# Kernel optimization log

Measured on AMD Instinct MI355X. Metric: run time of the kernel, lower is better.

The kernel has to match this reference:

```python
import jax, jax.numpy as jnp
import numpy as np

B, T, D, H, L = 8, 128, 400, 300, 45  # batch, max_length, 2*word_lstm_size, hidden, tag_count


def setup_inputs() -> dict:
    key = jax.random.key(0)
    ks = jax.random.split(key, 10)
    s = 0.05
    return {
        "cont_repr": jax.random.normal(ks[0], (B, T, D), jnp.float32),
        "root": jax.random.normal(ks[1], (1, 1, D), jnp.float32),
        "W1a": jax.random.normal(ks[2], (D, H), jnp.float32) * s,
        "W1b": jax.random.normal(ks[3], (D, H), jnp.float32) * s,
        "b1": jnp.zeros((H,), jnp.float32),
        "Wa": jax.random.normal(ks[4], (H, 1), jnp.float32) * s,
        "ba": jnp.zeros((1,), jnp.float32),
        "Wl": jax.random.normal(ks[5], (H, L), jnp.float32) * s,
        "bl": jnp.zeros((L,), jnp.float32),
        "sentence_lengths": jax.random.randint(ks[6], (B,), 0, T + 1),
        "desired_arcs": jax.random.randint(ks[7], (B, T), 0, T + 1),
        "desired_labels": jax.random.randint(ks[8], (B, T), 0, L),
        "use_desired_arcs": 1,
    }


def reference(cont_repr, root, W1a, W1b, b1, Wa, ba, Wl, bl,
              sentence_lengths, desired_arcs, desired_labels, use_desired_arcs):
    b, t, d = cont_repr.shape
    mask = (jnp.arange(t)[None, :] < sentence_lengths[:, None]).astype(cont_repr.dtype)  # [B,T]
    n_valid = jnp.maximum(mask.sum(), 1.0)

    # Dense(concat(tile_a, tile_b)) == tile_a @ W1a + tile_b @ W1b (exact same math,
    # avoids materializing the [B,T,T+1,2D] concat the TF graph builds).
    a_proj = jnp.einsum('btd,dh->bth', cont_repr, W1a)                     # [B,T,H]
    with_root = jnp.concatenate([jnp.broadcast_to(root, (b, 1, d)), cont_repr], axis=1)  # [B,T+1,D]
    b_proj = jnp.einsum('bsd,dh->bsh', with_root, W1b)                     # [B,T+1,H]
    h = jax.nn.relu(a_proj[:, :, None, :] + b_proj[:, None, :, :] + b1)    # [B,T,T+1,H]

    # UAS: arc scorer (units=1) over T+1 head candidates
    arc_logits = jnp.einsum('btsh,ho->btso', h, Wa)[..., 0] + ba[0]        # [B,T,T+1]
    predicted_arcs = jnp.argmax(arc_logits, axis=-1)                        # [B,T]
    arc_logp = jax.nn.log_softmax(arc_logits, axis=-1)
    arc_ce = -jnp.take_along_axis(arc_logp, desired_arcs[..., None], axis=-1)[..., 0]
    uas_loss = (arc_ce * mask).sum() / n_valid

    # LAS: gather pair repr at selected head, score labels
    sel = desired_arcs if use_desired_arcs else predicted_arcs             # [B,T]
    idx = jnp.broadcast_to(sel[:, :, None, None], (b, t, 1, h.shape[-1]))
    sel_h = jnp.take_along_axis(h, idx, axis=2)[:, :, 0, :]                # [B,T,H]
    lab_logits = jnp.einsum('bth,hl->btl', sel_h, Wl) + bl                 # [B,T,L]
    lab_logp = jax.nn.log_softmax(lab_logits, axis=-1)
    lab_ce = -jnp.take_along_axis(lab_logp, desired_labels[..., None], axis=-1)[..., 0]
    las_loss = (lab_ce * mask).sum() / n_valid

    return (uas_loss + las_loss) / 2
```

## Files before the change

kernel.cpp:

```cpp
#include <hip/hip_runtime.h>
#include <hip/hip_bf16.h>
#include <math.h>

#define BN 8
#define TT 128
#define DD 400
#define HH 300
#define LL 45
#define KH 200
#define SS 129
#define ALG_STRIDE 132
#define PADW 308

__global__ __launch_bounds__(640) void proj_kernel(
    const float* __restrict__ cont, const float* __restrict__ root,
    const float* __restrict__ W1a, const float* __restrict__ W1b,
    const float* __restrict__ b1,
    const int* __restrict__ slen,
    float* __restrict__ AP, float* __restrict__ BPX,
    float* __restrict__ accum)
{
    __shared__ float red[320][9];
    const int blk = blockIdx.x;
    const int tid = threadIdx.x;
    const int grp = tid / 320;
    const int h   = tid % 320;
    const int d0  = __builtin_amdgcn_readfirstlane(grp * KH);

    if (blk == 256) {
        if (tid == 0) accum[0] = 0.f;
        float acc = 0.f;
        if (h < HH) {
            const float* wp = W1b + (size_t)d0 * HH + h;
            for (int d = 0; d < KH; ++d)
                acc = fmaf(root[d0 + d], wp[(size_t)d * HH], acc);
        }
        if (grp == 1) red[h][0] = acc;
        __syncthreads();
        if (grp == 0 && h < HH) {
            const float v = acc + red[h][0];
            for (int bb = 0; bb < BN; ++bb)
                BPX[(size_t)bb * SS * HH + h] = v;
        }
        return;
    }

    const bool isA = (blk < 128);
    const int rb   = isA ? blk : blk - 128;
    const int row0 = rb * 8;
    if (isA) {
        const int lenb = slen[row0 >> 7];
        if ((row0 & 127) >= lenb) return;
    }

    const float* W    = isA ? W1a : W1b;
    const float* rows = cont + (size_t)row0 * DD + d0;

    float acc[8];
    #pragma unroll
    for (int r = 0; r < 8; ++r) acc[r] = 0.f;

    if (h < HH) {
        const float* wp = W + (size_t)d0 * HH + h;
        float w[8];
        #pragma unroll
        for (int k = 0; k < 8; ++k) w[k] = wp[(size_t)k * HH];
        for (int dc = 0; dc < KH; dc += 8) {
            float wn[8];
            if (dc + 8 < KH) {
                #pragma unroll
                for (int k = 0; k < 8; ++k) wn[k] = wp[(size_t)(dc + 8 + k) * HH];
            } else {
                #pragma unroll
                for (int k = 0; k < 8; ++k) wn[k] = 0.f;
            }
            #pragma unroll
            for (int r = 0; r < 8; ++r) {
                const float* rp = rows + r * DD + dc;
                #pragma unroll
                for (int k = 0; k < 8; ++k)
                    acc[r] = fmaf(rp[k], w[k], acc[r]);
            }
            #pragma unroll
            for (int k = 0; k < 8; ++k) w[k] = wn[k];
        }
    }

    if (grp == 1) {
        #pragma unroll
        for (int r = 0; r < 8; ++r) red[h][r] = acc[r];
    }
    __syncthreads();
    if (grp == 0 && h < HH) {
        if (isA) {
            const float bb = b1[h];
            float* dst = AP + (size_t)row0 * HH + h;
            #pragma unroll
            for (int r = 0; r < 8; ++r)
                dst[(size_t)r * HH] = acc[r] + red[h][r] + bb;
        } else {
            const int b = row0 >> 7, t = row0 & 127;
            float* dst = BPX + ((size_t)(b * SS + t + 1)) * HH + h;
            #pragma unroll
            for (int r = 0; r < 8; ++r)
                dst[(size_t)r * HH] = acc[r] + red[h][r];
        }
    }
}

__global__ __launch_bounds__(256) void arc_kernel(
    const float* __restrict__ AP, const float* __restrict__ BPX,
    const float* __restrict__ Wa, const int* __restrict__ slen,
    float* __restrict__ ALG)
{
    __shared__ float ap_s[8][PADW];
    __shared__ float bp_s[33][PADW];
    __shared__ float wa_s[PADW];

    const int blk = blockIdx.x;
    const int b  = blk >> 6;
    const int tt = (blk >> 2) & 15;
    const int sc = blk & 3;
    const int t0 = tt * 8;
    if (t0 >= slen[b]) return;

    const int tid  = threadIdx.x;
    const int lane = tid & 63;
    const int wave = tid >> 6;
    const int tl   = lane & 7;
    const int sl   = lane >> 3;
    const int s0   = sc * 32;

    {
        const float* apg = AP + (size_t)(b * TT + t0) * HH;
        for (int i = tid; i < 8 * HH; i += 256)
            ap_s[i / HH][i % HH] = apg[(i / HH) * HH + i % HH];
        const float* bpg = BPX + (size_t)(b * SS + s0) * HH;
        for (int i = tid; i < 33 * HH; i += 256)
            bp_s[i / HH][i % HH] = bpg[(i / HH) * HH + i % HH];
        for (int i = tid; i < HH; i += 256)
            wa_s[i] = Wa[i];
    }
    __syncthreads();

    const int s_local = wave * 8 + sl;
    const float* aprow = ap_s[tl];
    const float* bprow = bp_s[s_local];

    float acc = 0.f;
    #pragma unroll 5
    for (int hh = 0; hh < HH; hh += 4) {
        const float4 a4 = *(const float4*)&aprow[hh];
        const float4 p4 = *(const float4*)&bprow[hh];
        const float4 w4 = *(const float4*)&wa_s[hh];
        acc = fmaf(fmaxf(a4.x + p4.x, 0.f), w4.x, acc);
        acc = fmaf(fmaxf(a4.y + p4.y, 0.f), w4.y, acc);
        acc = fmaf(fmaxf(a4.z + p4.z, 0.f), w4.z, acc);
        acc = fmaf(fmaxf(a4.w + p4.w, 0.f), w4.w, acc);
    }
    ALG[(size_t)(b * TT + t0 + tl) * ALG_STRIDE + s0 + s_local] = acc;

    if (sc == 3 && wave == 0 && sl == 0) {
        const float* bpr = bp_s[32];
        float a2 = 0.f;
        #pragma unroll 5
        for (int hh = 0; hh < HH; hh += 4) {
            const float4 a4 = *(const float4*)&aprow[hh];
            const float4 p4 = *(const float4*)&bpr[hh];
            const float4 w4 = *(const float4*)&wa_s[hh];
            a2 = fmaf(fmaxf(a4.x + p4.x, 0.f), w4.x, a2);
            a2 = fmaf(fmaxf(a4.y + p4.y, 0.f), w4.y, a2);
            a2 = fmaf(fmaxf(a4.z + p4.z, 0.f), w4.z, a2);
            a2 = fmaf(fmaxf(a4.w + p4.w, 0.f), w4.w, a2);
        }
        ALG[(size_t)(b * TT + t0 + tl) * ALG_STRIDE + 128] = a2;
    }
}

__global__ __launch_bounds__(256) void smx_kernel(
    const float* __restrict__ AP, const float* __restrict__ BPX,
    const float* __restrict__ Wl, const float* __restrict__ bl,
    const float* __restrict__ ALG,
    const int* __restrict__ slen, const int* __restrict__ des_arcs,
    const int* __restrict__ des_labels, const int* __restrict__ use_des,
    float* __restrict__ accum)
{
    const int blk = blockIdx.x;
    const int b = blk >> 7, t = blk & 127;
    if (t >= slen[b]) return;
    const int tid  = threadIdx.x;
    const int lane = tid & 63;
    const int wave = tid >> 6;

    __shared__ float selh[HH];
    __shared__ float partial[4][64];
    __shared__ float arc_ce_s;
    __shared__ int   sel_s;

    if (wave == 0) {
        const float* lg = ALG + (size_t)blk * ALG_STRIDE;
        const float v0 = lg[lane];
        const float v1 = lg[64 + lane];
        const float v2 = (lane == 0) ? lg[128] : -INFINITY;

        float m = fmaxf(fmaxf(v0, v1), v2);
        #pragma unroll
        for (int off = 32; off; off >>= 1) m = fmaxf(m, __shfl_xor(m, off, 64));
        float e = __expf(v0 - m) + __expf(v1 - m) + ((lane == 0) ? __expf(v2 - m) : 0.f);
        #pragma unroll
        for (int off = 32; off; off >>= 1) e += __shfl_xor(e, off, 64);
        const float arc_lse = m + __logf(e);

        float bv = v0; int bi = lane;
        if (v1 > bv) { bv = v1; bi = 64 + lane; }
        if (lane == 0 && v2 > bv) { bv = v2; bi = 128; }
        #pragma unroll
        for (int off = 32; off; off >>= 1) {
            const float ov = __shfl_xor(bv, off, 64);
            const int   oi = __shfl_xor(bi, off, 64);
            if (ov > bv || (ov == bv && oi < bi)) { bv = ov; bi = oi; }
        }
        if (lane == 0) {
            const int da = des_arcs[b * TT + t];
            arc_ce_s = arc_lse - lg[da];
            sel_s = use_des[0] ? da : bi;
        }
    }
    __syncthreads();

    {
        const int sel = sel_s;
        const float* ap = AP + (size_t)blk * HH;
        const float* bp = BPX + (size_t)(b * SS + sel) * HH;
        for (int hh = tid; hh < HH; hh += 256)
            selh[hh] = fmaxf(ap[hh] + bp[hh], 0.f);
    }
    __syncthreads();

    {
        float p = 0.f;
        if (lane < LL) {
            const int h0 = wave * 75;
            #pragma unroll 5
            for (int j = 0; j < 75; ++j)
                p = fmaf(selh[h0 + j], Wl[(h0 + j) * LL + lane], p);
        }
        partial[wave][lane] = p;
    }
    __syncthreads();

    if (wave == 0) {
        float a = -INFINITY;
        if (lane < LL)
            a = bl[lane] + partial[0][lane] + partial[1][lane]
                         + partial[2][lane] + partial[3][lane];
        float lm = a;
        #pragma unroll
        for (int off = 32; off; off >>= 1) lm = fmaxf(lm, __shfl_xor(lm, off, 64));
        float le = (lane < LL) ? __expf(a - lm) : 0.f;
        #pragma unroll
        for (int off = 32; off; off >>= 1) le += __shfl_xor(le, off, 64);
        const float lab_lse = lm + __logf(le);

        const int dl = des_labels[b * TT + t];
        const float ldl = __shfl(a, dl, 64);
        if (lane == 0)
            atomicAdd(accum, arc_ce_s + (lab_lse - ldl));
    }
}

__global__ void finalize_kernel(const float* __restrict__ accum,
                                const int* __restrict__ slen,
                                float* __restrict__ out)
{
    if (threadIdx.x == 0) {
        int n = 0;
        for (int b = 0; b < BN; ++b) {
            int l = slen[b];
            if (l < 0) l = 0;
            if (l > TT) l = TT;
            n += l;
        }
        float nv = (float)n;
        if (nv < 1.f) nv = 1.f;
        out[0] = accum[0] / (2.f * nv);
    }
}

extern "C" void kernel_launch(void* const* d_in, const int* in_sizes, int n_in,
                              void* d_out, int out_size, void* d_ws, size_t ws_size,
                              hipStream_t stream) {
    const float* cont = (const float*)d_in[0];
    const float* root = (const float*)d_in[1];
    const float* W1a  = (const float*)d_in[2];
    const float* W1b  = (const float*)d_in[3];
    const float* b1   = (const float*)d_in[4];
    const float* Wa   = (const float*)d_in[5];
    const float* Wl   = (const float*)d_in[7];
    const float* bl   = (const float*)d_in[8];
    const int* slen   = (const int*)d_in[9];
    const int* darc   = (const int*)d_in[10];
    const int* dlab   = (const int*)d_in[11];
    const int* used   = (const int*)d_in[12];
    float* out = (float*)d_out;

    float* AP    = (float*)d_ws;
    float* BPX   = AP  + 1024 * HH;
    float* ALG   = BPX + BN * SS * HH;
    float* accum = ALG + 1024 * ALG_STRIDE;

    proj_kernel<<<257, 640, 0, stream>>>(cont, root, W1a, W1b, b1, slen, AP, BPX, accum);
    arc_kernel<<<512, 256, 0, stream>>>(AP, BPX, Wa, slen, ALG);
    smx_kernel<<<1024, 256, 0, stream>>>(AP, BPX, Wl, bl, ALG, slen, darc, dlab, used, accum);
    finalize_kernel<<<1, 64, 0, stream>>>(accum, slen, out);
}
```

Baseline: 47.11 us.

## Repartition projection kernel into more, smaller blocks without split-K reduction

Result: slower. 54.43 us (+15.5%).

```diff
diff --git a/kernel.cpp b/kernel.cpp
--- a/kernel.cpp
+++ b/kernel.cpp
@@ -7,12 +7,11 @@
 #define DD 400
 #define HH 300
 #define LL 45
-#define KH 200
 #define SS 129
 #define ALG_STRIDE 132
 #define PADW 308
 
-__global__ __launch_bounds__(640) void proj_kernel(
+__global__ __launch_bounds__(256) void proj_kernel(
     const float* __restrict__ cont, const float* __restrict__ root,
     const float* __restrict__ W1a, const float* __restrict__ W1b,
     const float* __restrict__ b1,
@@ -20,90 +19,85 @@
     float* __restrict__ AP, float* __restrict__ BPX,
     float* __restrict__ accum)
 {
-    __shared__ float red[320][9];
-    const int blk = blockIdx.x;
-    const int tid = threadIdx.x;
-    const int grp = tid / 320;
-    const int h   = tid % 320;
-    const int d0  = __builtin_amdgcn_readfirstlane(grp * KH);
-
-    if (blk == 256) {
+    const int tid  = threadIdx.x;
+    const int blk  = blockIdx.x;
+
+    if (blk == 1280) {
         if (tid == 0) accum[0] = 0.f;
-        float acc = 0.f;
-        if (h < HH) {
-            const float* wp = W1b + (size_t)d0 * HH + h;
-            for (int d = 0; d < KH; ++d)
-                acc = fmaf(root[d0 + d], wp[(size_t)d * HH], acc);
-        }
-        if (grp == 1) red[h][0] = acc;
-        __syncthreads();
-        if (grp == 0 && h < HH) {
-            const float v = acc + red[h][0];
+        for (int h = tid; h < HH; h += 256) {
+            float a0 = 0.f, a1 = 0.f, a2 = 0.f, a3 = 0.f;
+            const float* wp = W1b + h;
+            for (int d = 0; d < DD; d += 4) {
+                a0 = fmaf(root[d],     wp[(size_t)d * HH],           a0);
+                a1 = fmaf(root[d + 1], wp[(size_t)(d + 1) * HH],     a1);
+                a2 = fmaf(root[d + 2], wp[(size_t)(d + 2) * HH],     a2);
+                a3 = fmaf(root[d + 3], wp[(size_t)(d + 3) * HH],     a3);
+            }
+            const float v = (a0 + a1) + (a2 + a3);
+            #pragma unroll
             for (int bb = 0; bb < BN; ++bb)
                 BPX[(size_t)bb * SS * HH + h] = v;
         }
         return;
     }
 
-    const bool isA = (blk < 128);
-    const int rb   = isA ? blk : blk - 128;
+    const bool isA = (blk < 640);
+    const int q    = isA ? blk : blk - 640;
+    const int rb   = q / 5;
+    const int hc   = q % 5;
     const int row0 = rb * 8;
     if (isA) {
         const int lenb = slen[row0 >> 7];
         if ((row0 & 127) >= lenb) return;
     }
 
-    const float* W    = isA ? W1a : W1b;
-    const float* rows = cont + (size_t)row0 * DD + d0;
-
-    float acc[8];
+    const int lane = tid & 63;
+    const int wave = tid >> 6;
+    const int h    = hc * 64 + lane;
+    const bool hok = (h < HH);
+    const int hs   = hok ? h : 0;
+
+    const int roff = __builtin_amdgcn_readfirstlane((row0 + wave * 2) * DD);
+    const float* x0 = cont + roff;
+    const float* x1 = x0 + DD;
+
+    const float* wp = (isA ? W1a : W1b) + hs;
+
+    float acc0 = 0.f, acc1 = 0.f;
+    float w[8];
     #pragma unroll
-    for (int r = 0; r < 8; ++r) acc[r] = 0.f;
-
-    if (h < HH) {
-        const float* wp = W + (size_t)d0 * HH + h;
-        float w[8];
-        #pragma unroll
-        for (int k = 0; k < 8; ++k) w[k] = wp[(size_t)k * HH];
-        for (int dc = 0; dc < KH; dc += 8) {
-            float wn[8];
-            if (dc + 8 < KH) {
-                #pragma unroll
-                for (int k = 0; k < 8; ++k) wn[k] = wp[(size_t)(dc + 8 + k) * HH];
-            } else {
-                #pragma unroll
-                for (int k = 0; k < 8; ++k) wn[k] = 0.f;
-            }
+    for (int k = 0; k < 8; ++k) w[k] = wp[(size_t)k * HH];
+
+    for (int dc = 0; dc < DD; dc += 8) {
+        float wn[8];
+        if (dc + 8 < DD) {
             #pragma unroll
-            for (int r = 0; r < 8; ++r) {
-                const float* rp = rows + r * DD + dc;
-                #pragma unroll
-                for (int k = 0; k < 8; ++k)
-                    acc[r] = fmaf(rp[k], w[k], acc[r]);
-            }
+            for (int k = 0; k < 8; ++k) wn[k] = wp[(size_t)(dc + 8 + k) * HH];
+        } else {
             #pragma unroll
-            for (int k = 0; k < 8; ++k) w[k] = wn[k];
-        }
-    }
-
-    if (grp == 1) {
-        #pragma unroll
-        for (int r = 0; r < 8; ++r) red[h][r] = acc[r];
-    }
-    __syncthreads();
-    if (grp == 0 && h < HH) {
+            for (int k = 0; k < 8; ++k) wn[k] = 0.f;
+        }
+        #pragma unroll
+        for (int k = 0; k < 8; ++k) {
+            acc0 = fmaf(x0[dc + k], w[k], acc0);
+            acc1 = fmaf(x1[dc + k], w[k], acc1);
+        }
+        #pragma unroll
+        for (int k = 0; k < 8; ++k) w[k] = wn[k];
+    }
+
+    if (hok) {
+        const int t = (row0 & 127) + wave * 2;
         if (isA) {
             const float bb = b1[h];
-            float* dst = AP + (size_t)row0 * HH + h;
-            #pragma unroll
-            for (int r = 0; r < 8; ++r)
-                dst[(size_t)r * HH] = acc[r] + red[h][r] + bb;
+            float* dst = AP + (size_t)(row0 + wave * 2) * HH + h;
+            dst[0]  = acc0 + bb;
+            dst[HH] = acc1 + bb;
         } else {
-            const int b = row0 >> 7, t = row0 & 127;
+            const int b = row0 >> 7;
             float* dst = BPX + ((size_t)(b * SS + t + 1)) * HH + h;
-            #pragma unroll
-            for (int r = 0; r < 8; ++r)
-                dst[(size_t)r * HH] = acc[r] + red[h][r];
+            dst[0]  = acc0;
+            dst[HH] = acc1;
         }
     }
 }
@@ -309,7 +303,7 @@
     float* ALG   = BPX + BN * SS * HH;
     float* accum = ALG + 1024 * ALG_STRIDE;
 
-    proj_kernel<<<257, 640, 0, stream>>>(cont, root, W1a, W1b, b1, slen, AP, BPX, accum);
+    proj_kernel<<<1281, 256, 0, stream>>>(cont, root, W1a, W1b, b1, slen, AP, BPX, accum);
     arc_kernel<<<512, 256, 0, stream>>>(AP, BPX, Wa, slen, ALG);
     smx_kernel<<<1024, 256, 0, stream>>>(AP, BPX, Wl, bl, ALG, slen, darc, dlab, used, accum);
     finalize_kernel<<<1, 64, 0, stream>>>(accum, slen, out);
```

## Stage input rows in LDS and drop split-K reduction in projection kernel

Applied to the files above, without the earlier changes.

Result: slower. 58.12 us (+23.4%).

```diff
diff --git a/kernel.cpp b/kernel.cpp
--- a/kernel.cpp
+++ b/kernel.cpp
@@ -7,12 +7,11 @@
 #define DD 400
 #define HH 300
 #define LL 45
-#define KH 200
 #define SS 129
 #define ALG_STRIDE 132
 #define PADW 308
 
-__global__ __launch_bounds__(640) void proj_kernel(
+__global__ __launch_bounds__(320) void proj_kernel(
     const float* __restrict__ cont, const float* __restrict__ root,
     const float* __restrict__ W1a, const float* __restrict__ W1b,
     const float* __restrict__ b1,
@@ -20,91 +19,102 @@
     float* __restrict__ AP, float* __restrict__ BPX,
     float* __restrict__ accum)
 {
-    __shared__ float red[320][9];
+    __shared__ float rows_s[8 * DD];
     const int blk = blockIdx.x;
     const int tid = threadIdx.x;
-    const int grp = tid / 320;
-    const int h   = tid % 320;
-    const int d0  = __builtin_amdgcn_readfirstlane(grp * KH);
+    const int h   = tid;
+    const bool hok = (h < HH);
 
     if (blk == 256) {
         if (tid == 0) accum[0] = 0.f;
-        float acc = 0.f;
-        if (h < HH) {
-            const float* wp = W1b + (size_t)d0 * HH + h;
-            for (int d = 0; d < KH; ++d)
-                acc = fmaf(root[d0 + d], wp[(size_t)d * HH], acc);
-        }
-        if (grp == 1) red[h][0] = acc;
+        for (int i = tid; i < DD; i += 320) rows_s[i] = root[i];
         __syncthreads();
-        if (grp == 0 && h < HH) {
-            const float v = acc + red[h][0];
+        if (hok) {
+            const float* wp = W1b + h;
+            float acc = 0.f;
+            float w[8];
+            #pragma unroll
+            for (int k = 0; k < 8; ++k) w[k] = wp[(size_t)k * HH];
+            for (int dc = 0; dc < DD; dc += 8) {
+                float wn[8];
+                if (dc + 8 < DD) {
+                    #pragma unroll
+                    for (int k = 0; k < 8; ++k) wn[k] = wp[(size_t)(dc + 8 + k) * HH];
+                } else {
+                    #pragma unroll
+                    for (int k = 0; k < 8; ++k) wn[k] = 0.f;
+                }
+                const float4 ra = *(const float4*)&rows_s[dc];
+                const float4 rb = *(const float4*)&rows_s[dc + 4];
+                acc = fmaf(ra.x, w[0], acc); acc = fmaf(ra.y, w[1], acc);
+                acc = fmaf(ra.z, w[2], acc); acc = fmaf(ra.w, w[3], acc);
+                acc = fmaf(rb.x, w[4], acc); acc = fmaf(rb.y, w[5], acc);
+                acc = fmaf(rb.z, w[6], acc); acc = fmaf(rb.w, w[7], acc);
+                #pragma unroll
+                for (int k = 0; k < 8; ++k) w[k] = wn[k];
+            }
+            #pragma unroll
             for (int bb = 0; bb < BN; ++bb)
-                BPX[(size_t)bb * SS * HH + h] = v;
+                BPX[(size_t)bb * SS * HH + h] = acc;
         }
         return;
     }
 
     const bool isA = (blk < 128);
-    const int rb   = isA ? blk : blk - 128;
-    const int row0 = rb * 8;
+    const int u    = isA ? blk : blk - 128;
+    const int row0 = u * 8;
     if (isA) {
-        const int lenb = slen[row0 >> 7];
-        if ((row0 & 127) >= lenb) return;
-    }
-
-    const float* W    = isA ? W1a : W1b;
-    const float* rows = cont + (size_t)row0 * DD + d0;
-
+        if ((row0 & 127) >= slen[row0 >> 7]) return;
+    }
+
+    {
+        const float* src = cont + (size_t)row0 * DD;
+        for (int i = tid; i < 8 * DD; i += 320) rows_s[i] = src[i];
+    }
+    __syncthreads();
+    if (!hok) return;
+
+    const float* wp = (isA ? W1a : W1b) + h;
     float acc[8];
     #pragma unroll
     for (int r = 0; r < 8; ++r) acc[r] = 0.f;
 
-    if (h < HH) {
-        const float* wp = W + (size_t)d0 * HH + h;
-        float w[8];
-        #pragma unroll
-        for (int k = 0; k < 8; ++k) w[k] = wp[(size_t)k * HH];
-        for (int dc = 0; dc < KH; dc += 8) {
-            float wn[8];
-            if (dc + 8 < KH) {
-                #pragma unroll
-                for (int k = 0; k < 8; ++k) wn[k] = wp[(size_t)(dc + 8 + k) * HH];
-            } else {
-                #pragma unroll
-                for (int k = 0; k < 8; ++k) wn[k] = 0.f;
-            }
+    float w[8];
+    #pragma unroll
+    for (int k = 0; k < 8; ++k) w[k] = wp[(size_t)k * HH];
+
+    for (int dc = 0; dc < DD; dc += 8) {
+        float wn[8];
+        if (dc + 8 < DD) {
             #pragma unroll
-            for (int r = 0; r < 8; ++r) {
-                const float* rp = rows + r * DD + dc;
-                #pragma unroll
-                for (int k = 0; k < 8; ++k)
-                    acc[r] = fmaf(rp[k], w[k], acc[r]);
-            }
+            for (int k = 0; k < 8; ++k) wn[k] = wp[(size_t)(dc + 8 + k) * HH];
+        } else {
             #pragma unroll
-            for (int k = 0; k < 8; ++k) w[k] = wn[k];
-        }
-    }
-
-    if (grp == 1) {
-        #pragma unroll
-        for (int r = 0; r < 8; ++r) red[h][r] = acc[r];
-    }
-    __syncthreads();
-    if (grp == 0 && h < HH) {
-        if (isA) {
-            const float bb = b1[h];
-            float* dst = AP + (size_t)row0 * HH + h;
-            #pragma unroll
-            for (int r = 0; r < 8; ++r)
-                dst[(size_t)r * HH] = acc[r] + red[h][r] + bb;
-        } else {
-            const int b = row0 >> 7, t = row0 & 127;
-            float* dst = BPX + ((size_t)(b * SS + t + 1)) * HH + h;
-            #pragma unroll
-            for (int r = 0; r < 8; ++r)
-                dst[(size_t)r * HH] = acc[r] + red[h][r];
-        }
+            for (int k = 0; k < 8; ++k) wn[k] = 0.f;
+        }
+        #pragma unroll
+        for (int r = 0; r < 8; ++r) {
+            const float4 ra = *(const float4*)&rows_s[r * DD + dc];
+            const float4 rb = *(const float4*)&rows_s[r * DD + dc + 4];
+            acc[r] = fmaf(ra.x, w[0], acc[r]); acc[r] = fmaf(ra.y, w[1], acc[r]);
+            acc[r] = fmaf(ra.z, w[2], acc[r]); acc[r] = fmaf(ra.w, w[3], acc[r]);
+            acc[r] = fmaf(rb.x, w[4], acc[r]); acc[r] = fmaf(rb.y, w[5], acc[r]);
+            acc[r] = fmaf(rb.z, w[6], acc[r]); acc[r] = fmaf(rb.w, w[7], acc[r]);
+        }
+        #pragma unroll
+        for (int k = 0; k < 8; ++k) w[k] = wn[k];
+    }
+
+    if (isA) {
+        const float bb = b1[h];
+        float* dst = AP + (size_t)row0 * HH + h;
+        #pragma unroll
+        for (int r = 0; r < 8; ++r) dst[(size_t)r * HH] = acc[r] + bb;
+    } else {
+        const int b = row0 >> 7, t = row0 & 127;
+        float* dst = BPX + ((size_t)(b * SS + t + 1)) * HH + h;
+        #pragma unroll
+        for (int r = 0; r < 8; ++r) dst[(size_t)r * HH] = acc[r];
     }
 }
 
@@ -134,10 +144,10 @@
     {
         const float* apg = AP + (size_t)(b * TT + t0) * HH;
         for (int i = tid; i < 8 * HH; i += 256)
-            ap_s[i / HH][i % HH] = apg[(i / HH) * HH + i % HH];
+            ap_s[i / HH][i % HH] = apg[i];
         const float* bpg = BPX + (size_t)(b * SS + s0) * HH;
         for (int i = tid; i < 33 * HH; i += 256)
-            bp_s[i / HH][i % HH] = bpg[(i / HH) * HH + i % HH];
+            bp_s[i / HH][i % HH] = bpg[i];
         for (int i = tid; i < HH; i += 256)
             wa_s[i] = Wa[i];
     }
@@ -309,7 +319,7 @@
     float* ALG   = BPX + BN * SS * HH;
     float* accum = ALG + 1024 * ALG_STRIDE;
 
-    proj_kernel<<<257, 640, 0, stream>>>(cont, root, W1a, W1b, b1, slen, AP, BPX, accum);
+    proj_kernel<<<257, 320, 0, stream>>>(cont, root, W1a, W1b, b1, slen, AP, BPX, accum);
     arc_kernel<<<512, 256, 0, stream>>>(AP, BPX, Wa, slen, ALG);
     smx_kernel<<<1024, 256, 0, stream>>>(AP, BPX, Wl, bl, ALG, slen, darc, dlab, used, accum);
     finalize_kernel<<<1, 64, 0, stream>>>(accum, slen, out);
```
